# Kernel tuning notes

Measured on AMD Instinct MI355X. Metric: run time of the kernel, lower is better.

The kernel has to match this reference:

```python
import jax, jax.numpy as jnp
import numpy as np

WS = 7            # window size
HEADS = 4
DIM = 128         # hidden_dim
HEAD_DIM = 128    # wrapper passes head_dim=hidden_dim (faithful to source)
INNER = HEADS * HEAD_DIM   # 512
MLP = 4 * DIM
PATCH = 4
DISP = WS // 2
NEG = -1e9


def _ln(x, g, b, eps=1e-5):
    m = jnp.mean(x, -1, keepdims=True)
    v = jnp.mean((x - m) ** 2, -1, keepdims=True)
    return (x - m) * jax.lax.rsqrt(v + eps) * g + b


_coords = np.stack(np.meshgrid(np.arange(WS), np.arange(WS), indexing='ij'), -1).reshape(-1, 2)
REL_IDX = jnp.asarray(_coords[None] - _coords[:, None] + WS - 1)  # (ws^2, ws^2, 2)


def _build_masks():
    n = WS * WS
    ul = np.zeros((n, n), np.float32)
    ul[-DISP * WS:, : -DISP * WS] = NEG
    ul[: -DISP * WS, -DISP * WS:] = NEG
    lr = np.zeros((WS, WS, WS, WS), np.float32)
    lr[:, -DISP:, :, : -DISP] = NEG
    lr[:, : -DISP, :, -DISP:] = NEG
    return jnp.asarray(ul), jnp.asarray(lr.reshape(n, n))

UL_MASK, LR_MASK = _build_masks()


def _win_attn(x, w_qkv, pos, w_o, b_o, shifted):
    b, H, W, _ = x.shape
    if shifted:
        x = jnp.roll(x, (-DISP, -DISP), axis=(1, 2))
    nh, nw = H // WS, W // WS
    qkv = x @ w_qkv  # (b, H, W, 3*INNER)

    def to_win(t):  # -> (b, heads, n_windows, ws*ws, head_dim)
        t = t.reshape(b, nh, WS, nw, WS, HEADS, HEAD_DIM)
        return t.transpose(0, 5, 1, 3, 2, 4, 6).reshape(b, HEADS, nh * nw, WS * WS, HEAD_DIM)

    q, k, v = map(to_win, jnp.split(qkv, 3, axis=-1))
    dots = jnp.einsum('bhwid,bhwjd->bhwij', q, k) * (HEAD_DIM ** -0.5)
    dots = dots + pos[REL_IDX[..., 0], REL_IDX[..., 1]]  # shared across heads (berniwal)
    if shifted:
        dots = dots.at[:, :, -nw:].add(UL_MASK)
        dots = dots.at[:, :, nw - 1::nw].add(LR_MASK)
    attn = jax.nn.softmax(dots, axis=-1)
    out = jnp.einsum('bhwij,bhwjd->bhwid', attn, v)
    out = out.reshape(b, HEADS, nh, nw, WS, WS, HEAD_DIM).transpose(0, 2, 4, 3, 5, 1, 6)
    out = out.reshape(b, H, W, INNER) @ w_o + b_o
    if shifted:
        out = jnp.roll(out, (DISP, DISP), axis=(1, 2))
    return out


def _block(x, ga1, be1, w_qkv, pos, w_o, b_o, ga2, be2, w1, b1, w2, b2, shifted):
    x = x + _win_attn(_ln(x, ga1, be1), w_qkv, pos, w_o, b_o, shifted)
    h = jax.nn.gelu(_ln(x, ga2, be2) @ w1 + b1, approximate=False) @ w2 + b2
    return x + h


def _patch_embed(x, w, b):  # Unfold(patch) + Linear, channel-major feature order
    B, C, H, W = x.shape
    nh, nw = H // PATCH, W // PATCH
    x = x.reshape(B, C, nh, PATCH, nw, PATCH).transpose(0, 2, 4, 1, 3, 5)
    return x.reshape(B, nh, nw, C * PATCH * PATCH) @ w + b


def setup_inputs() -> dict:
    key = jax.random.key(0)
    ks = iter(jax.random.split(key, 48))

    def nrm(shape, s=0.02):
        return jax.random.normal(next(ks), shape, dtype=jnp.float32) * s

    inp = {'x': jax.random.normal(next(ks), (32, 3, 224, 224), dtype=jnp.float32)}
    inp['w_pe'] = nrm((3 * PATCH * PATCH, DIM))
    inp['b_pe'] = jnp.zeros((DIM,), jnp.float32)
    for s in ('a', 'b'):
        inp['ga1_' + s] = jnp.ones((DIM,), jnp.float32)
        inp['be1_' + s] = jnp.zeros((DIM,), jnp.float32)
        inp['w_qkv_' + s] = nrm((DIM, 3 * INNER))
        inp['pos_' + s] = nrm((2 * WS - 1, 2 * WS - 1), 1.0)
        inp['w_o_' + s] = nrm((INNER, DIM))
        inp['b_o_' + s] = jnp.zeros((DIM,), jnp.float32)
        inp['ga2_' + s] = jnp.ones((DIM,), jnp.float32)
        inp['be2_' + s] = jnp.zeros((DIM,), jnp.float32)
        inp['w_m1_' + s] = nrm((DIM, MLP))
        inp['b_m1_' + s] = jnp.zeros((MLP,), jnp.float32)
        inp['w_m2_' + s] = nrm((MLP, DIM))
        inp['b_m2_' + s] = jnp.zeros((DIM,), jnp.float32)
    return inp


def reference(x, w_pe, b_pe,
              ga1_a, be1_a, w_qkv_a, pos_a, w_o_a, b_o_a, ga2_a, be2_a, w_m1_a, b_m1_a, w_m2_a, b_m2_a,
              ga1_b, be1_b, w_qkv_b, pos_b, w_o_b, b_o_b, ga2_b, be2_b, w_m1_b, b_m1_b, w_m2_b, b_m2_b):
    h = _patch_embed(x, w_pe, b_pe)  # (B, 56, 56, DIM)
    h = _block(h, ga1_a, be1_a, w_qkv_a, pos_a, w_o_a, b_o_a, ga2_a, be2_a, w_m1_a, b_m1_a, w_m2_a, b_m2_a, False)
    h = _block(h, ga1_b, be1_b, w_qkv_b, pos_b, w_o_b, b_o_b, ga2_b, be2_b, w_m1_b, b_m1_b, w_m2_b, b_m2_b, True)
    return h
```

## Files before the change

kernel.cpp:

```cpp
#include <hip/hip_runtime.h>

typedef __attribute__((ext_vector_type(8))) short bf16x8;
typedef __attribute__((ext_vector_type(4))) short bf16x4;
typedef __attribute__((ext_vector_type(4))) float f32x4;

#define MFMA16(a, b, c) __builtin_amdgcn_mfma_f32_16x16x32_bf16(a, b, c, 0, 0, 0)

static __device__ __forceinline__ short f2bf(float f) {
    union { float f; unsigned u; } x; x.f = f;
    unsigned r = x.u + 0x7FFFu + ((x.u >> 16) & 1u);
    return (short)(r >> 16);
}

static __device__ __forceinline__ void gload16(const void* g, void* l) {
    __builtin_amdgcn_global_load_lds((const __attribute__((address_space(1))) void*)g,
                                     (__attribute__((address_space(3))) void*)l, 16, 0, 0);
}

__global__ void convT_kernel(const float* __restrict__ in, short* __restrict__ out, int K, int N) {
    int idx = blockIdx.x * 256 + threadIdx.x;
    if (idx < K * N) {
        int k = idx % K, n = idx / K;
        out[idx] = f2bf(in[(size_t)k * N + n]);
    }
}

__global__ void tabgen_kernel(const float* __restrict__ pos_a, const float* __restrict__ pos_b,
                              float* __restrict__ tab) {
    int v = blockIdx.x;
    const float* pos = (v == 0) ? pos_a : pos_b;
    for (int e = threadIdx.x; e < 4096; e += 256) {
        int row = e >> 6, key = e & 63;
        float val;
        if (key >= 49) val = -1e9f;
        else if (row >= 49) val = 0.f;
        else {
            int qi = row / 7, qj = row - qi * 7, ki = key / 7, kj = key - ki * 7;
            val = pos[(ki - qi + 6) * 13 + (kj - qj + 6)];
            if (v >= 1) {
                bool wh7 = (v - 1) & 2, ww7 = (v - 1) & 1;
                if (wh7 && ((qi >= 4) != (ki >= 4))) val += -1e9f;
                if (ww7 && ((qj >= 4) != (kj >= 4))) val += -1e9f;
            }
        }
        tab[v * 4096 + e] = val;
    }
}

__global__ __launch_bounds__(256) void patchln_kernel(const float* __restrict__ x,
                                                      const float* __restrict__ w,
                                                      const float* __restrict__ bias,
                                                      const float* __restrict__ g,
                                                      const float* __restrict__ bta,
                                                      float* __restrict__ out,
                                                      short* __restrict__ xn) {
    __shared__ float s_in[2][48];
    __shared__ float red[2][2][2];
    const int tid = threadIdx.x;
    const int half = tid >> 7, c = tid & 127;
    const int winh = (tid >> 6) & 1, lane = tid & 63;
    const int t = blockIdx.x * 2 + half;
    const int b = t / 3136, rem = t - b * 3136;
    const int hp = rem / 56, wp = rem - hp * 56;
    if (c < 48) {
        int cin = c >> 4, py = (c >> 2) & 3, px = c & 3;
        s_in[half][c] = x[((size_t)(b * 3 + cin) * 224 + hp * 4 + py) * 224 + wp * 4 + px];
    }
    __syncthreads();
    float acc = bias[c];
#pragma unroll
    for (int k = 0; k < 48; ++k) acc += s_in[half][k] * w[k * 128 + c];
    out[(size_t)t * 128 + c] = acc;
    float s1 = acc, s2 = acc * acc;
#pragma unroll
    for (int o = 32; o > 0; o >>= 1) { s1 += __shfl_xor(s1, o); s2 += __shfl_xor(s2, o); }
    if (lane == 0) { red[half][winh][0] = s1; red[half][winh][1] = s2; }
    __syncthreads();
    s1 = red[half][0][0] + red[half][1][0];
    s2 = red[half][0][1] + red[half][1][1];
    float mean = s1 * (1.f / 128.f);
    float var = s2 * (1.f / 128.f) - mean * mean;
    float rstd = rsqrtf(var + 1e-5f);
    xn[(size_t)t * 128 + c] = f2bf((acc - mean) * rstd * g[c] + bta[c]);
}

template <int SHIFTED>
__global__ __launch_bounds__(256, 3) void attn_kernel(const short* __restrict__ xn,
                                                      const short* __restrict__ wqkvT,
                                                      const float* __restrict__ tab,
                                                      const short* __restrict__ zpad,
                                                      short* __restrict__ aout) {
    __shared__ short smem[24576];
    short* s_x = smem;
    short* s_q = smem + 8192;
    short* s_k = smem + 16384;
    short* s_vT = smem + 8192;
    short* s_p = smem + 16384;

    const int tid = threadIdx.x;
    const int wid = tid >> 6, lane = tid & 63;
    const int l15 = lane & 15, l4 = lane >> 4, klo = l4 * 8;
    const int bid = blockIdx.x;
    const int win = bid & 63, head = (bid >> 6) & 3, b = bid >> 8;
    const int wh = win >> 3, ww = win & 7;

#pragma unroll
    for (int it = 0; it < 4; ++it) {
        int slot = it * 256 + tid;
        int row = slot >> 4, scol = slot & 15;
        int colb = (scol * 16) ^ ((row & 7) << 4);
        const char* g;
        if (row < 49) {
            int wi = row / 7, wj = row - wi * 7;
            int hh = wh * 7 + wi, wp = ww * 7 + wj;
            if (SHIFTED) { hh += 3; if (hh >= 56) hh -= 56; wp += 3; if (wp >= 56) wp -= 56; }
            int t = (b * 56 + hh) * 56 + wp;
            g = (const char*)(xn + (size_t)t * 128) + colb;
        } else {
            g = (const char*)zpad + colb;
        }
        gload16(g, (char*)smem + (it * 256 + wid * 64) * 16);
    }
    __syncthreads();

    const f32x4 zero4 = {0.f, 0.f, 0.f, 0.f};

    {
        const short* Wq = wqkvT + (size_t)(head * 128) * 128;
        const short* Wk = wqkvT + (size_t)(512 + head * 128) * 128;
        f32x4 aq[2][4], ak[2][4];
#pragma unroll
        for (int mw = 0; mw < 2; ++mw)
#pragma unroll
            for (int j = 0; j < 4; ++j) { aq[mw][j] = zero4; ak[mw][j] = zero4; }
#pragma unroll
        for (int k0 = 0; k0 < 4; ++k0) {
            bf16x8 bx[4], awq[2], awk[2];
#pragma unroll
            for (int j = 0; j < 4; ++j) {
                int row = j * 16 + l15;
                bx[j] = *(const bf16x8*)((const char*)s_x + row * 256 + ((k0 * 64 + l4 * 16) ^ ((row & 7) << 4)));
            }
#pragma unroll
            for (int mw = 0; mw < 2; ++mw) {
                awq[mw] = *(const bf16x8*)(Wq + (size_t)(wid * 32 + mw * 16 + l15) * 128 + k0 * 32 + klo);
                awk[mw] = *(const bf16x8*)(Wk + (size_t)(wid * 32 + mw * 16 + l15) * 128 + k0 * 32 + klo);
            }
            __builtin_amdgcn_s_setprio(1);
#pragma unroll
            for (int mw = 0; mw < 2; ++mw)
#pragma unroll
                for (int j = 0; j < 4; ++j) {
                    aq[mw][j] = MFMA16(awq[mw], bx[j], aq[mw][j]);
                    ak[mw][j] = MFMA16(awk[mw], bx[j], ak[mw][j]);
                }
            __builtin_amdgcn_s_setprio(0);
        }
#pragma unroll
        for (int mw = 0; mw < 2; ++mw)
#pragma unroll
            for (int j = 0; j < 4; ++j) {
                bf16x4 pq, pk;
#pragma unroll
                for (int r = 0; r < 4; ++r) { pq[r] = f2bf(aq[mw][j][r]); pk[r] = f2bf(ak[mw][j][r]); }
                int row = j * 16 + l15;
                int colb = (wid * 64 + mw * 32 + l4 * 8) ^ ((row & 7) << 4);
                *(bf16x4*)((char*)s_q + row * 256 + colb) = pq;
                *(bf16x4*)((char*)s_k + row * 256 + colb) = pk;
            }
    }
    __syncthreads();

    const int qrow = wid * 16 + l15;
    f32x4 dt[4];
#pragma unroll
    for (int m = 0; m < 4; ++m) dt[m] = zero4;
#pragma unroll
    for (int k0 = 0; k0 < 4; ++k0) {
        bf16x8 bq = *(const bf16x8*)((const char*)s_q + qrow * 256 + ((k0 * 64 + l4 * 16) ^ ((qrow & 7) << 4)));
        __builtin_amdgcn_s_setprio(1);
#pragma unroll
        for (int m = 0; m < 4; ++m) {
            int krow = m * 16 + l15;
            bf16x8 akf = *(const bf16x8*)((const char*)s_k + krow * 256 + ((k0 * 64 + l4 * 16) ^ ((krow & 7) << 4)));
            dt[m] = MFMA16(akf, bq, dt[m]);
        }
        __builtin_amdgcn_s_setprio(0);
    }
    __syncthreads();

    const int variant = SHIFTED ? (1 + ((wh == 7) ? 2 : 0) + ((ww == 7) ? 1 : 0)) : 0;
    const float* tv = tab + variant * 4096 + qrow * 64;
    const float SC = 0.08838834764831845f;
    float p[4][4];
    float mx = -3.0e38f;
#pragma unroll
    for (int m = 0; m < 4; ++m) {
        f32x4 tb = *(const f32x4*)(tv + m * 16 + l4 * 4);
#pragma unroll
        for (int r = 0; r < 4; ++r) {
            float d = dt[m][r] * SC + tb[r];
            p[m][r] = d;
            mx = fmaxf(mx, d);
        }
    }
    mx = fmaxf(mx, __shfl_xor(mx, 16));
    mx = fmaxf(mx, __shfl_xor(mx, 32));
    float sum = 0.f;
#pragma unroll
    for (int m = 0; m < 4; ++m)
#pragma unroll
        for (int r = 0; r < 4; ++r) { p[m][r] = __expf(p[m][r] - mx); sum += p[m][r]; }
    sum += __shfl_xor(sum, 16);
    sum += __shfl_xor(sum, 32);
    float inv = 1.f / sum;
#pragma unroll
    for (int m = 0; m < 4; ++m) {
        bf16x4 pv;
#pragma unroll
        for (int r = 0; r < 4; ++r) pv[r] = f2bf(p[m][r] * inv);
        *(bf16x4*)((char*)s_p + qrow * 128 + ((m * 32 + l4 * 8) ^ ((qrow & 7) << 4))) = pv;
    }

    {
        const short* Wv = wqkvT + (size_t)(1024 + head * 128) * 128;
        f32x4 acc[4][2];
#pragma unroll
        for (int m = 0; m < 4; ++m)
#pragma unroll
            for (int n = 0; n < 2; ++n) acc[m][n] = zero4;
#pragma unroll
        for (int k0 = 0; k0 < 4; ++k0) {
            bf16x8 ax[4], bw[2];
#pragma unroll
            for (int m = 0; m < 4; ++m) {
                int row = m * 16 + l15;
                ax[m] = *(const bf16x8*)((const char*)s_x + row * 256 + ((k0 * 64 + l4 * 16) ^ ((row & 7) << 4)));
            }
#pragma unroll
            for (int n = 0; n < 2; ++n)
                bw[n] = *(const bf16x8*)(Wv + (size_t)(wid * 32 + n * 16 + l15) * 128 + k0 * 32 + klo);
            __builtin_amdgcn_s_setprio(1);
#pragma unroll
            for (int m = 0; m < 4; ++m)
#pragma unroll
                for (int n = 0; n < 2; ++n) acc[m][n] = MFMA16(ax[m], bw[n], acc[m][n]);
            __builtin_amdgcn_s_setprio(0);
        }
#pragma unroll
        for (int m = 0; m < 4; ++m)
#pragma unroll
            for (int n = 0; n < 2; ++n) {
                bf16x4 pv;
#pragma unroll
                for (int r = 0; r < 4; ++r) pv[r] = f2bf(acc[m][n][r]);
                int hd = wid * 32 + n * 16 + l15;
                int colb = (m * 32 + l4 * 8) ^ ((hd & 7) << 4);
                *(bf16x4*)((char*)s_vT + hd * 128 + colb) = pv;
            }
    }
    __syncthreads();

    f32x4 o[4][2];
#pragma unroll
    for (int m = 0; m < 4; ++m)
#pragma unroll
        for (int n = 0; n < 2; ++n) o[m][n] = zero4;
#pragma unroll
    for (int k0 = 0; k0 < 2; ++k0) {
        bf16x8 ap[4], bv[2];
#pragma unroll
        for (int m = 0; m < 4; ++m) {
            int row = m * 16 + l15;
            ap[m] = *(const bf16x8*)((const char*)s_p + row * 128 + ((k0 * 64 + l4 * 16) ^ ((row & 7) << 4)));
        }
#pragma unroll
        for (int n = 0; n < 2; ++n) {
            int hd = wid * 32 + n * 16 + l15;
            bv[n] = *(const bf16x8*)((const char*)s_vT + hd * 128 + ((k0 * 64 + l4 * 16) ^ ((hd & 7) << 4)));
        }
        __builtin_amdgcn_s_setprio(1);
#pragma unroll
        for (int m = 0; m < 4; ++m)
#pragma unroll
            for (int n = 0; n < 2; ++n) o[m][n] = MFMA16(ap[m], bv[n], o[m][n]);
        __builtin_amdgcn_s_setprio(0);
    }
#pragma unroll
    for (int m = 0; m < 4; ++m) {
#pragma unroll
        for (int r = 0; r < 4; ++r) {
            int rl = m * 16 + l4 * 4 + r;
            if (rl < 49) {
                int wi = rl / 7, wj = rl - wi * 7;
                int hh = wh * 7 + wi, wp = ww * 7 + wj;
                if (SHIFTED) { hh += 3; if (hh >= 56) hh -= 56; wp += 3; if (wp >= 56) wp -= 56; }
                size_t t = (size_t)(b * 56 + hh) * 56 + wp;
                aout[t * 512 + head * 128 + wid * 32 + l15] = f2bf(o[m][0][r]);
                aout[t * 512 + head * 128 + wid * 32 + 16 + l15] = f2bf(o[m][1][r]);
            }
        }
    }
}

template <int K, int MODE>
__global__ __launch_bounds__(256, 2) void gemm2_kernel(const short* __restrict__ A,
                                                       const short* __restrict__ BT,
                                                       const float* __restrict__ bias,
                                                       const float* __restrict__ resid,
                                                       const float* __restrict__ g,
                                                       const float* __restrict__ bta,
                                                       float* __restrict__ outf,
                                                       short* __restrict__ outb,
                                                       int Ntot) {
    __shared__ char smem[32768];
    short* s_a = (short*)smem;
    short* s_b = (short*)(smem + 16384);
    float* red = (float*)smem;

    const int tid = threadIdx.x, wid = tid >> 6, lane = tid & 63;
    const int wr = wid >> 1, wc = wid & 1;
    const int l15 = lane & 15, l4 = lane >> 4;
    const int m0 = blockIdx.x * 128;
    const int nb0 = blockIdx.y * 128;

    const f32x4 zero4 = {0.f, 0.f, 0.f, 0.f};
    f32x4 acc[4][4];
#pragma unroll
    for (int m = 0; m < 4; ++m)
#pragma unroll
        for (int n = 0; n < 4; ++n) acc[m][n] = zero4;

    for (int kc = 0; kc < K / 64; ++kc) {
#pragma unroll
        for (int it = 0; it < 4; ++it) {
            int slot = it * 256 + tid;
            int row = slot >> 3, scol = slot & 7;
            int colb = (scol * 16) ^ ((row & 7) << 4);
            gload16((const char*)(A + (size_t)(m0 + row) * K + kc * 64) + colb,
                    (char*)smem + (it * 256 + wid * 64) * 16);
        }
#pragma unroll
        for (int it = 0; it < 4; ++it) {
            int slot = it * 256 + tid;
            int row = slot >> 3, scol = slot & 7;
            int colb = (scol * 16) ^ ((row & 7) << 4);
            gload16((const char*)(BT + (size_t)(nb0 + row) * K + kc * 64) + colb,
                    (char*)smem + 16384 + (it * 256 + wid * 64) * 16);
        }
        __syncthreads();
#pragma unroll
        for (int ks = 0; ks < 2; ++ks) {
            bf16x8 a[4], bfr[4];
#pragma unroll
            for (int m = 0; m < 4; ++m) {
                int row = wr * 64 + m * 16 + l15;
                a[m] = *(const bf16x8*)((const char*)s_a + row * 128 + ((ks * 64 + l4 * 16) ^ ((row & 7) << 4)));
            }
#pragma unroll
            for (int n = 0; n < 4; ++n) {
                int row = wc * 64 + n * 16 + l15;
                bfr[n] = *(const bf16x8*)((const char*)s_b + row * 128 + ((ks * 64 + l4 * 16) ^ ((row & 7) << 4)));
            }
            __builtin_amdgcn_s_setprio(1);
#pragma unroll
            for (int m = 0; m < 4; ++m)
#pragma unroll
                for (int n = 0; n < 4; ++n) acc[m][n] = MFMA16(a[m], bfr[n], acc[m][n]);
            __builtin_amdgcn_s_setprio(0);
        }
        __syncthreads();
    }

    float bv[4];
#pragma unroll
    for (int n = 0; n < 4; ++n) bv[n] = bias[nb0 + wc * 64 + n * 16 + l15];

    if (MODE == 0) {
#pragma unroll
        for (int m = 0; m < 4; ++m)
#pragma unroll
            for (int r = 0; r < 4; ++r) {
                int row = m0 + wr * 64 + m * 16 + l4 * 4 + r;
#pragma unroll
                for (int n = 0; n < 4; ++n) {
                    int col = nb0 + wc * 64 + n * 16 + l15;
                    float v = acc[m][n][r] + bv[n];
                    v = 0.5f * v * (1.f + erff(v * 0.70710678118f));
                    outb[(size_t)row * Ntot + col] = f2bf(v);
                }
            }
        return;
    }

    float s1[4][4], s2[4][4];
#pragma unroll
    for (int m = 0; m < 4; ++m)
#pragma unroll
        for (int r = 0; r < 4; ++r) {
            int row = m0 + wr * 64 + m * 16 + l4 * 4 + r;
            float a1 = 0.f, a2 = 0.f;
#pragma unroll
            for (int n = 0; n < 4; ++n) {
                int col = wc * 64 + n * 16 + l15;
                float v = acc[m][n][r] + bv[n] + resid[(size_t)row * 128 + col];
                acc[m][n][r] = v;
                a1 += v; a2 += v * v;
            }
            s1[m][r] = a1; s2[m][r] = a2;
        }

    if (MODE == 1) {
#pragma unroll
        for (int m = 0; m < 4; ++m)
#pragma unroll
            for (int r = 0; r < 4; ++r) {
#pragma unroll
                for (int o = 1; o < 16; o <<= 1) {
                    s1[m][r] += __shfl_xor(s1[m][r], o);
                    s2[m][r] += __shfl_xor(s2[m][r], o);
                }
            }
        __syncthreads();
#pragma unroll
        for (int m = 0; m < 4; ++m)
#pragma unroll
            for (int r = 0; r < 4; ++r) {
                if (l15 == m * 4 + r) {
                    int lrow = wr * 64 + m * 16 + l4 * 4 + r;
                    red[lrow * 4 + wc * 2] = s1[m][r];
                    red[lrow * 4 + wc * 2 + 1] = s2[m][r];
                }
            }
        __syncthreads();
    }

#pragma unroll
    for (int m = 0; m < 4; ++m)
#pragma unroll
        for (int r = 0; r < 4; ++r) {
            int lrow = wr * 64 + m * 16 + l4 * 4 + r;
            int row = m0 + lrow;
            float mean = 0.f, rstd = 0.f;
            if (MODE == 1) {
                float t1 = red[lrow * 4] + red[lrow * 4 + 2];
                float t2 = red[lrow * 4 + 1] + red[lrow * 4 + 3];
                mean = t1 * (1.f / 128.f);
                float var = t2 * (1.f / 128.f) - mean * mean;
                rstd = rsqrtf(var + 1e-5f);
            }
#pragma unroll
            for (int n = 0; n < 4; ++n) {
                int col = wc * 64 + n * 16 + l15;
                float v = acc[m][n][r];
                outf[(size_t)row * 128 + col] = v;
                if (MODE == 1)
                    outb[(size_t)row * 128 + col] = f2bf((v - mean) * rstd * g[col] + bta[col]);
            }
        }
}

extern "C" void kernel_launch(void* const* d_in, const int* in_sizes, int n_in,
                              void* d_out, int out_size, void* d_ws, size_t ws_size,
                              hipStream_t stream) {
    const float* x = (const float*)d_in[0];
    const float* w_pe = (const float*)d_in[1];
    const float* b_pe = (const float*)d_in[2];
    const float* P[24];
    for (int i = 0; i < 24; ++i) P[i] = (const float*)d_in[3 + i];

    float* out = (float*)d_out;
    const size_t TOK = 100352;

    short* xn = (short*)d_ws;
    short* abuf = xn + TOK * 128;
    short* wqkv = abuf + TOK * 512;
    short* wo = wqkv + 196608;
    short* wm1 = wo + 65536;
    short* wm2 = wm1 + 65536;
    float* tab = (float*)(wm2 + 65536);
    short* zpad = (short*)(tab + 5 * 4096);

    hipMemsetAsync(zpad, 0, 256, stream);
    tabgen_kernel<<<5, 256, 0, stream>>>(P[3], P[15], tab);

    patchln_kernel<<<50176, 256, 0, stream>>>(x, w_pe, b_pe, P[0], P[1], out, xn);

    for (int s = 0; s < 2; ++s) {
        convT_kernel<<<768, 256, 0, stream>>>(P[s * 12 + 2], wqkv, 128, 1536);
        convT_kernel<<<256, 256, 0, stream>>>(P[s * 12 + 4], wo, 512, 128);
        convT_kernel<<<256, 256, 0, stream>>>(P[s * 12 + 8], wm1, 128, 512);
        convT_kernel<<<256, 256, 0, stream>>>(P[s * 12 + 10], wm2, 512, 128);

        if (s == 0)
            attn_kernel<0><<<8192, 256, 0, stream>>>(xn, wqkv, tab, zpad, abuf);
        else
            attn_kernel<1><<<8192, 256, 0, stream>>>(xn, wqkv, tab, zpad, abuf);

        gemm2_kernel<512, 1><<<dim3(784, 1), 256, 0, stream>>>(
            abuf, wo, P[s * 12 + 5], out, P[s * 12 + 6], P[s * 12 + 7], out, xn, 128);

        gemm2_kernel<128, 0><<<dim3(784, 4), 256, 0, stream>>>(
            xn, wm1, P[s * 12 + 9], nullptr, nullptr, nullptr, nullptr, abuf, 512);

        if (s == 0)
            gemm2_kernel<512, 1><<<dim3(784, 1), 256, 0, stream>>>(
                abuf, wm2, P[11], out, P[12], P[13], out, xn, 128);
        else
            gemm2_kernel<512, 2><<<dim3(784, 1), 256, 0, stream>>>(
                abuf, wm2, P[23], out, nullptr, nullptr, out, nullptr, 128);
    }
}
```

Measured before the change: 624.2 us.

## Double-buffer GEMM A tiles, load weights directly, drop attention LDS staging of X

```diff
diff --git a/kernel.cpp b/kernel.cpp
--- a/kernel.cpp
+++ b/kernel.cpp
@@ -3,6 +3,7 @@
 typedef __attribute__((ext_vector_type(8))) short bf16x8;
 typedef __attribute__((ext_vector_type(4))) short bf16x4;
 typedef __attribute__((ext_vector_type(4))) float f32x4;
+typedef __attribute__((ext_vector_type(2))) unsigned u32x2;
 
 #define MFMA16(a, b, c) __builtin_amdgcn_mfma_f32_16x16x32_bf16(a, b, c, 0, 0, 0)
 
@@ -10,6 +11,12 @@
     union { float f; unsigned u; } x; x.f = f;
     unsigned r = x.u + 0x7FFFu + ((x.u >> 16) & 1u);
     return (short)(r >> 16);
+}
+
+static __device__ __forceinline__ unsigned cvtpk(float lo, float hi) {
+    unsigned r;
+    asm("v_cvt_pk_bf16_f32 %0, %1, %2" : "=v"(r) : "v"(lo), "v"(hi));
+    return r;
 }
 
 static __device__ __forceinline__ void gload16(const void* g, void* l) {
@@ -85,17 +92,15 @@
 }
 
 template <int SHIFTED>
-__global__ __launch_bounds__(256, 3) void attn_kernel(const short* __restrict__ xn,
+__global__ __launch_bounds__(256, 4) void attn_kernel(const short* __restrict__ xn,
                                                       const short* __restrict__ wqkvT,
                                                       const float* __restrict__ tab,
-                                                      const short* __restrict__ zpad,
                                                       short* __restrict__ aout) {
-    __shared__ short smem[24576];
-    short* s_x = smem;
-    short* s_q = smem + 8192;
-    short* s_k = smem + 16384;
-    short* s_vT = smem + 8192;
-    short* s_p = smem + 16384;
+    __shared__ short smem[16384];
+    short* s_q = smem;
+    short* s_k = smem + 8192;
+    short* s_vT = smem;
+    short* s_p = smem + 8192;
 
     const int tid = threadIdx.x;
     const int wid = tid >> 6, lane = tid & 63;
@@ -104,69 +109,50 @@
     const int win = bid & 63, head = (bid >> 6) & 3, b = bid >> 8;
     const int wh = win >> 3, ww = win & 7;
 
-#pragma unroll
-    for (int it = 0; it < 4; ++it) {
-        int slot = it * 256 + tid;
-        int row = slot >> 4, scol = slot & 15;
-        int colb = (scol * 16) ^ ((row & 7) << 4);
-        const char* g;
-        if (row < 49) {
-            int wi = row / 7, wj = row - wi * 7;
-            int hh = wh * 7 + wi, wp = ww * 7 + wj;
-            if (SHIFTED) { hh += 3; if (hh >= 56) hh -= 56; wp += 3; if (wp >= 56) wp -= 56; }
-            int t = (b * 56 + hh) * 56 + wp;
-            g = (const char*)(xn + (size_t)t * 128) + colb;
-        } else {
-            g = (const char*)zpad + colb;
-        }
-        gload16(g, (char*)smem + (it * 256 + wid * 64) * 16);
-    }
-    __syncthreads();
+    int trow[4];
+#pragma unroll
+    for (int j = 0; j < 4; ++j) {
+        int r = j * 16 + l15; r = (r > 48) ? 48 : r;
+        int wi = (r * 37) >> 8, wj = r - wi * 7;
+        int hh = wh * 7 + wi, wp = ww * 7 + wj;
+        if (SHIFTED) { hh += 3; if (hh >= 56) hh -= 56; wp += 3; if (wp >= 56) wp -= 56; }
+        trow[j] = (b * 56 + hh) * 56 + wp;
+    }
 
     const f32x4 zero4 = {0.f, 0.f, 0.f, 0.f};
 
-    {
-        const short* Wq = wqkvT + (size_t)(head * 128) * 128;
-        const short* Wk = wqkvT + (size_t)(512 + head * 128) * 128;
-        f32x4 aq[2][4], ak[2][4];
+#pragma unroll
+    for (int pr = 0; pr < 2; ++pr) {
+        const short* W = wqkvT + (size_t)(pr * 512 + head * 128) * 128;
+        f32x4 ac[2][4];
 #pragma unroll
         for (int mw = 0; mw < 2; ++mw)
 #pragma unroll
-            for (int j = 0; j < 4; ++j) { aq[mw][j] = zero4; ak[mw][j] = zero4; }
+            for (int j = 0; j < 4; ++j) ac[mw][j] = zero4;
 #pragma unroll
         for (int k0 = 0; k0 < 4; ++k0) {
-            bf16x8 bx[4], awq[2], awk[2];
+            bf16x8 bx[4], aw[2];
+#pragma unroll
+            for (int j = 0; j < 4; ++j)
+                bx[j] = *(const bf16x8*)(xn + (size_t)trow[j] * 128 + k0 * 32 + klo);
+#pragma unroll
+            for (int mw = 0; mw < 2; ++mw)
+                aw[mw] = *(const bf16x8*)(W + (size_t)(wid * 32 + mw * 16 + l15) * 128 + k0 * 32 + klo);
+            __builtin_amdgcn_s_setprio(1);
+#pragma unroll
+            for (int mw = 0; mw < 2; ++mw)
+#pragma unroll
+                for (int j = 0; j < 4; ++j) ac[mw][j] = MFMA16(aw[mw], bx[j], ac[mw][j]);
+            __builtin_amdgcn_s_setprio(0);
+        }
+        short* dst = pr ? s_k : s_q;
+#pragma unroll
+        for (int mw = 0; mw < 2; ++mw)
 #pragma unroll
             for (int j = 0; j < 4; ++j) {
+                u32x2 pv = { cvtpk(ac[mw][j][0], ac[mw][j][1]), cvtpk(ac[mw][j][2], ac[mw][j][3]) };
                 int row = j * 16 + l15;
-                bx[j] = *(const bf16x8*)((const char*)s_x + row * 256 + ((k0 * 64 + l4 * 16) ^ ((row & 7) << 4)));
-            }
-#pragma unroll
-            for (int mw = 0; mw < 2; ++mw) {
-                awq[mw] = *(const bf16x8*)(Wq + (size_t)(wid * 32 + mw * 16 + l15) * 128 + k0 * 32 + klo);
-                awk[mw] = *(const bf16x8*)(Wk + (size_t)(wid * 32 + mw * 16 + l15) * 128 + k0 * 32 + klo);
-            }
-            __builtin_amdgcn_s_setprio(1);
-#pragma unroll
-            for (int mw = 0; mw < 2; ++mw)
-#pragma unroll
-                for (int j = 0; j < 4; ++j) {
-                    aq[mw][j] = MFMA16(awq[mw], bx[j], aq[mw][j]);
-                    ak[mw][j] = MFMA16(awk[mw], bx[j], ak[mw][j]);
-                }
-            __builtin_amdgcn_s_setprio(0);
-        }
-#pragma unroll
-        for (int mw = 0; mw < 2; ++mw)
-#pragma unroll
-            for (int j = 0; j < 4; ++j) {
-                bf16x4 pq, pk;
-#pragma unroll
-                for (int r = 0; r < 4; ++r) { pq[r] = f2bf(aq[mw][j][r]); pk[r] = f2bf(ak[mw][j][r]); }
-                int row = j * 16 + l15;
-                int colb = (wid * 64 + mw * 32 + l4 * 8) ^ ((row & 7) << 4);
-                *(bf16x4*)((char*)s_q + row * 256 + colb) = pq;
-                *(bf16x4*)((char*)s_k + row * 256 + colb) = pk;
+                *(u32x2*)((char*)dst + row * 256 + ((wid * 64 + mw * 32 + l4 * 8) ^ ((row & 7) << 4))) = pv;
             }
     }
     __syncthreads();
@@ -216,10 +202,8 @@
     float inv = 1.f / sum;
 #pragma unroll
     for (int m = 0; m < 4; ++m) {
-        bf16x4 pv;
-#pragma unroll
-        for (int r = 0; r < 4; ++r) pv[r] = f2bf(p[m][r] * inv);
-        *(bf16x4*)((char*)s_p + qrow * 128 + ((m * 32 + l4 * 8) ^ ((qrow & 7) << 4))) = pv;
+        u32x2 pv = { cvtpk(p[m][0] * inv, p[m][1] * inv), cvtpk(p[m][2] * inv, p[m][3] * inv) };
+        *(u32x2*)((char*)s_p + qrow * 128 + ((m * 32 + l4 * 8) ^ ((qrow & 7) << 4))) = pv;
     }
 
     {
@@ -233,10 +217,8 @@
         for (int k0 = 0; k0 < 4; ++k0) {
             bf16x8 ax[4], bw[2];
 #pragma unroll
-            for (int m = 0; m < 4; ++m) {
-                int row = m * 16 + l15;
-                ax[m] = *(const bf16x8*)((const char*)s_x + row * 256 + ((k0 * 64 + l4 * 16) ^ ((row & 7) << 4)));
-            }
+            for (int m = 0; m < 4; ++m)
+                ax[m] = *(const bf16x8*)(xn + (size_t)trow[m] * 128 + k0 * 32 + klo);
 #pragma unroll
             for (int n = 0; n < 2; ++n)
                 bw[n] = *(const bf16x8*)(Wv + (size_t)(wid * 32 + n * 16 + l15) * 128 + k0 * 32 + klo);
@@ -251,12 +233,9 @@
         for (int m = 0; m < 4; ++m)
 #pragma unroll
             for (int n = 0; n < 2; ++n) {
-                bf16x4 pv;
-#pragma unroll
-                for (int r = 0; r < 4; ++r) pv[r] = f2bf(acc[m][n][r]);
+                u32x2 pv = { cvtpk(acc[m][n][0], acc[m][n][1]), cvtpk(acc[m][n][2], acc[m][n][3]) };
                 int hd = wid * 32 + n * 16 + l15;
-                int colb = (m * 32 + l4 * 8) ^ ((hd & 7) << 4);
-                *(bf16x4*)((char*)s_vT + hd * 128 + colb) = pv;
+                *(u32x2*)((char*)s_vT + hd * 128 + ((m * 32 + l4 * 8) ^ ((hd & 7) << 4))) = pv;
             }
     }
     __syncthreads();
@@ -292,7 +271,7 @@
         for (int r = 0; r < 4; ++r) {
             int rl = m * 16 + l4 * 4 + r;
             if (rl < 49) {
-                int wi = rl / 7, wj = rl - wi * 7;
+                int wi = (rl * 37) >> 8, wj = rl - wi * 7;
                 int hh = wh * 7 + wi, wp = ww * 7 + wj;
                 if (SHIFTED) { hh += 3; if (hh >= 56) hh -= 56; wp += 3; if (wp >= 56) wp -= 56; }
                 size_t t = (size_t)(b * 56 + hh) * 56 + wp;
@@ -304,7 +283,7 @@
 }
 
 template <int K, int MODE>
-__global__ __launch_bounds__(256, 2) void gemm2_kernel(const short* __restrict__ A,
+__global__ __launch_bounds__(256, 3) void gemm3_kernel(const short* __restrict__ A,
                                                        const short* __restrict__ BT,
                                                        const float* __restrict__ bias,
                                                        const float* __restrict__ resid,
@@ -314,62 +293,65 @@
                                                        short* __restrict__ outb,
                                                        int Ntot) {
     __shared__ char smem[32768];
-    short* s_a = (short*)smem;
-    short* s_b = (short*)(smem + 16384);
     float* red = (float*)smem;
 
     const int tid = threadIdx.x, wid = tid >> 6, lane = tid & 63;
     const int wr = wid >> 1, wc = wid & 1;
-    const int l15 = lane & 15, l4 = lane >> 4;
+    const int l15 = lane & 15, l4 = lane >> 4, klo = l4 * 8;
     const int m0 = blockIdx.x * 128;
     const int nb0 = blockIdx.y * 128;
 
-    const f32x4 zero4 = {0.f, 0.f, 0.f, 0.f};
-    f32x4 acc[4][4];
-#pragma unroll
-    for (int m = 0; m < 4; ++m)
-#pragma unroll
-        for (int n = 0; n < 4; ++n) acc[m][n] = zero4;
-
-    for (int kc = 0; kc < K / 64; ++kc) {
+    auto stage = [&](int kc, int bi) {
 #pragma unroll
         for (int it = 0; it < 4; ++it) {
             int slot = it * 256 + tid;
             int row = slot >> 3, scol = slot & 7;
             int colb = (scol * 16) ^ ((row & 7) << 4);
             gload16((const char*)(A + (size_t)(m0 + row) * K + kc * 64) + colb,
-                    (char*)smem + (it * 256 + wid * 64) * 16);
-        }
-#pragma unroll
-        for (int it = 0; it < 4; ++it) {
-            int slot = it * 256 + tid;
-            int row = slot >> 3, scol = slot & 7;
-            int colb = (scol * 16) ^ ((row & 7) << 4);
-            gload16((const char*)(BT + (size_t)(nb0 + row) * K + kc * 64) + colb,
-                    (char*)smem + 16384 + (it * 256 + wid * 64) * 16);
-        }
-        __syncthreads();
+                    (char*)smem + bi * 16384 + (it * 256 + wid * 64) * 16);
+        }
+    };
+
+    const f32x4 zero4 = {0.f, 0.f, 0.f, 0.f};
+    f32x4 acc[4][4];
+#pragma unroll
+    for (int m = 0; m < 4; ++m)
+#pragma unroll
+        for (int n = 0; n < 4; ++n) acc[m][n] = zero4;
+
+    stage(0, 0);
+    const int KC = K / 64;
+#pragma unroll
+    for (int kc = 0; kc < KC; ++kc) {
+        asm volatile("s_waitcnt vmcnt(0)" ::: "memory");
+        __builtin_amdgcn_s_barrier();
+        __builtin_amdgcn_sched_barrier(0);
+        bf16x8 bfr[2][4];
+#pragma unroll
+        for (int ks = 0; ks < 2; ++ks)
+#pragma unroll
+            for (int n = 0; n < 4; ++n)
+                bfr[ks][n] = *(const bf16x8*)(BT + (size_t)(nb0 + wc * 64 + n * 16 + l15) * K + kc * 64 + ks * 32 + klo);
+        if (kc + 1 < KC) stage(kc + 1, (kc + 1) & 1);
+        const char* buf = (const char*)smem + (kc & 1) * 16384;
 #pragma unroll
         for (int ks = 0; ks < 2; ++ks) {
-            bf16x8 a[4], bfr[4];
+            bf16x8 a[4];
 #pragma unroll
             for (int m = 0; m < 4; ++m) {
                 int row = wr * 64 + m * 16 + l15;
-                a[m] = *(const bf16x8*)((const char*)s_a + row * 128 + ((ks * 64 + l4 * 16) ^ ((row & 7) << 4)));
-            }
-#pragma unroll
-            for (int n = 0; n < 4; ++n) {
-                int row = wc * 64 + n * 16 + l15;
-                bfr[n] = *(const bf16x8*)((const char*)s_b + row * 128 + ((ks * 64 + l4 * 16) ^ ((row & 7) << 4)));
+                a[m] = *(const bf16x8*)(buf + row * 128 + ((ks * 64 + l4 * 16) ^ ((row & 7) << 4)));
             }
             __builtin_amdgcn_s_setprio(1);
 #pragma unroll
             for (int m = 0; m < 4; ++m)
 #pragma unroll
-                for (int n = 0; n < 4; ++n) acc[m][n] = MFMA16(a[m], bfr[n], acc[m][n]);
+                for (int n = 0; n < 4; ++n) acc[m][n] = MFMA16(a[m], bfr[ks][n], acc[m][n]);
             __builtin_amdgcn_s_setprio(0);
         }
-        __syncthreads();
+        asm volatile("s_waitcnt lgkmcnt(0)" ::: "memory");
+        __builtin_amdgcn_sched_barrier(0);
+        __builtin_amdgcn_s_barrier();
     }
 
     float bv[4];
@@ -479,9 +461,7 @@
     short* wm1 = wo + 65536;
     short* wm2 = wm1 + 65536;
     float* tab = (float*)(wm2 + 65536);
-    short* zpad = (short*)(tab + 5 * 4096);
-
-    hipMemsetAsync(zpad, 0, 256, stream);
+
     tabgen_kernel<<<5, 256, 0, stream>>>(P[3], P[15], tab);
 
     patchln_kernel<<<50176, 256, 0, stream>>>(x, w_pe, b_pe, P[0], P[1], out, xn);
@@ -493,21 +473,21 @@
         convT_kernel<<<256, 256, 0, stream>>>(P[s * 12 + 10], wm2, 512, 128);
 
         if (s == 0)
-            attn_kernel<0><<<8192, 256, 0, stream>>>(xn, wqkv, tab, zpad, abuf);
+            attn_kernel<0><<<8192, 256, 0, stream>>>(xn, wqkv, tab, abuf);
         else
-            attn_kernel<1><<<8192, 256, 0, stream>>>(xn, wqkv, tab, zpad, abuf);
-
-        gemm2_kernel<512, 1><<<dim3(784, 1), 256, 0, stream>>>(
+            attn_kernel<1><<<8192, 256, 0, stream>>>(xn, wqkv, tab, abuf);
+
+        gemm3_kernel<512, 1><<<dim3(784, 1), 256, 0, stream>>>(
             abuf, wo, P[s * 12 + 5], out, P[s * 12 + 6], P[s * 12 + 7], out, xn, 128);
 
-        gemm2_kernel<128, 0><<<dim3(784, 4), 256, 0, stream>>>(
+        gemm3_kernel<128, 0><<<dim3(784, 4), 256, 0, stream>>>(
             xn, wm1, P[s * 12 + 9], nullptr, nullptr, nullptr, nullptr, abuf, 512);
 
         if (s == 0)
-            gemm2_kernel<512, 1><<<dim3(784, 1), 256, 0, stream>>>(
+            gemm3_kernel<512, 1><<<dim3(784, 1), 256, 0, stream>>>(
                 abuf, wm2, P[11], out, P[12], P[13], out, xn, 128);
         else
-            gemm2_kernel<512, 2><<<dim3(784, 1), 256, 0, stream>>>(
+            gemm3_kernel<512, 2><<<dim3(784, 1), 256, 0, stream>>>(
                 abuf, wm2, P[23], out, nullptr, nullptr, out, nullptr, 128);
     }
 }
```

After: 932.3 us. +49.4%, slower.
